# Optimization experiments

Measured on AMD Instinct MI355X. Metric: run time of the kernel, lower is better.

Reference implementation:

```python
import jax, jax.numpy as jnp
import numpy as np

B, NMAX, H, C, HID = 256, 512, 256, 64, 512
NEG = jnp.float32(-1e9)

def setup_inputs() -> dict:
    key = jax.random.key(0)
    ks = jax.random.split(key, 12)
    s_in = 1.0 / np.sqrt(2 * H + C)
    s_h = 1.0 / np.sqrt(HID)
    return {
        "nodes_hv": jax.random.normal(ks[0], (B, NMAX, H), jnp.float32),
        "class_cond": jax.random.normal(ks[1], (B, C), jnp.float32),
        "W1": jax.random.normal(ks[2], (2 * H + C, HID), jnp.float32) * s_in,
        "b1": jnp.zeros((HID,), jnp.float32),
        "W2": jax.random.normal(ks[3], (HID, HID), jnp.float32) * s_h,
        "b2": jnp.zeros((HID,), jnp.float32),
        "W3": jax.random.normal(ks[4], (HID, 1), jnp.float32) * s_h,
        "b3": jnp.zeros((1,), jnp.float32),
        "dirns": jax.random.randint(ks[5], (B,), 0, 2, jnp.int32),
        "node_counts": jax.random.randint(ks[6], (B,), NMAX // 2 + 1, NMAX, jnp.int32),
        "dests": jax.random.randint(ks[7], (B,), 0, NMAX // 2, jnp.int32),
    }

def reference(nodes_hv, class_cond, W1, b1, W2, b2, W3, b3, dirns, node_counts, dests):
    Bb, Nmax, Hh = nodes_hv.shape
    D = Nmax - 1  # padded number of candidate destinations
    # per-graph newest node embedding: hv[b, n_b - 1]
    src_idx = (node_counts - 1).astype(jnp.int32)
    src_embed = jnp.take_along_axis(nodes_hv, src_idx[:, None, None], axis=1)  # [B,1,H]
    src_b = jnp.broadcast_to(src_embed, (Bb, D, Hh))
    cand = nodes_hv[:, :D, :]  # candidate (old-node) embeddings, padded
    # dirn == 1: edge new->old, so (src_side, dest_side) = (cand, new); else (new, cand)
    dirn1 = (dirns == 1)[:, None, None]
    side_a = jnp.where(dirn1, cand, src_b)
    side_b = jnp.where(dirn1, src_b, cand)
    cc = jnp.broadcast_to(class_cond[:, None, :], (Bb, D, class_cond.shape[-1]))
    x = jnp.concatenate([side_a, side_b, cc], axis=2)  # [B, D, 2H+C]
    h = jax.nn.relu(jnp.einsum("bdi,ih->bdh", x, W1) + b1)
    h = jax.nn.relu(jnp.einsum("bdi,ih->bdh", h, W2) + b2)
    scores = (jnp.einsum("bdi,io->bdo", h, W3) + b3)[..., 0]  # [B, D]
    # ragged validity: graph b has n_b - 1 candidates
    valid = jnp.arange(D)[None, :] < (node_counts - 1)[:, None]
    scores = jnp.where(valid, scores, NEG)
    logp = jax.nn.log_softmax(scores, axis=1)
    loss = -jnp.take_along_axis(logp, dests[:, None].astype(jnp.int32), axis=1)[:, 0]  # [B]
    return loss
```

## Files before the change

kernel.cpp:

```cpp
#include <hip/hip_runtime.h>
#include <math.h>

#define BB    256
#define NMAX  512
#define HH    256
#define CC    64
#define HID   512
#define NEGV  -1000000000.0f
#define MT    64
#define NW    8
#define SA_LD 264
#define TILE  512
#define KSTR  (32 * TILE)

typedef __attribute__((ext_vector_type(8))) short short8;
typedef __attribute__((ext_vector_type(4))) float floatx4;

__device__ inline ushort f2bf(float x) {
    __bf16 b = (__bf16)x;
    return __builtin_bit_cast(ushort, b);
}

__global__ __launch_bounds__(512) void prep_kernel(
    const float* __restrict__ W1, const float* __restrict__ W2,
    ushort* __restrict__ Wt1s, ushort* __restrict__ Wt2s,
    const float* __restrict__ nodes_hv, const float* __restrict__ class_cond,
    const float* __restrict__ b1,
    const int* __restrict__ dirns, const int* __restrict__ node_counts,
    float* __restrict__ v_ws)
{
    const int blk = blockIdx.x;
    const int t = threadIdx.x;

    __shared__ float s_conv[32][68];
    __shared__ float s_src[HH];
    __shared__ float s_cc[CC];

    if (blk < 256) {
        const float* W = (blk < 128) ? W1 : W2;
        ushort* out    = (blk < 128) ? Wt1s : Wt2s;
        const int bb  = blk & 127;
        const int kb  = bb >> 3, ntg = bb & 7;

        if (t < 256) {
            const int kl = t >> 3, nn = (t & 7) * 8;
            const float* src = W + (size_t)(kb * 32 + kl) * HID + ntg * 64 + nn;
            *(float4*)&s_conv[kl][nn]     = *(const float4*)src;
            *(float4*)&s_conv[kl][nn + 4] = *(const float4*)(src + 4);
        }
        __syncthreads();

        if (t < 256) {
            const int ntl = t >> 6, ls = t & 63;
            const int qs = ls >> 4, l15s = ls & 15;
            short8 o;
            #pragma unroll
            for (int j = 0; j < 8; ++j)
                o[j] = (short)f2bf(s_conv[qs * 8 + j][ntl * 16 + l15s]);
            const int nt = ntg * 4 + ntl;
            *(short8*)(out + ((size_t)(kb * 32 + nt)) * TILE + ls * 8) = o;
        }
    } else {
        const int b = blk - 256;
        const int nc   = node_counts[b];
        const int dirn = dirns[b];
        const int src_idx = nc - 1;

        if (t < HH) s_src[t] = nodes_hv[((size_t)b * NMAX + src_idx) * HH + t];
        else if (t < HH + CC) s_cc[t - HH] = class_cond[b * CC + (t - HH)];
        __syncthreads();

        const int srcoff = (dirn == 1) ? HH : 0;

        const int j = t;
        float acc0 = b1[j];

        #pragma unroll 8
        for (int r = 0; r < HH; ++r)
            acc0 += s_src[r] * W1[(size_t)(srcoff + r) * HID + j];
        #pragma unroll 8
        for (int c = 0; c < CC; ++c)
            acc0 += s_cc[c] * W1[(size_t)(2 * HH + c) * HID + j];

        v_ws[b * HID + j] = acc0;
    }
}

__global__ __launch_bounds__(512, 4) void mlp2(
    const float* __restrict__ nodes_hv,
    const ushort* __restrict__ Wt1s, const ushort* __restrict__ Wt2s,
    const float* __restrict__ b2, const float* __restrict__ W3,
    const float* __restrict__ b3,
    const int* __restrict__ dirns, const int* __restrict__ node_counts,
    const float* __restrict__ v_ws, float* __restrict__ scores)
{
    const int b  = blockIdx.y;
    const int d0 = blockIdx.x * MT;
    const int t  = threadIdx.x;
    const int lane = t & 63, wv = t >> 6;
    const int l15 = lane & 15, q = lane >> 4;

    __shared__ ushort s_u[32768];

    const int nc = node_counts[b];

    if (d0 >= nc - 1) {
        if (t < MT) scores[b * NMAX + d0 + t] = NEGV;
        return;
    }

    const int kb0 = (dirns[b] == 1) ? 0 : 8;

    {
        const float4* src4 = (const float4*)nodes_hv + ((size_t)b * NMAX + d0) * (HH / 4);
        #pragma unroll
        for (int i = 0; i < (MT * HH / 4) / 512; ++i) {
            int idx = t + i * 512;
            int row = idx >> 6, c4 = idx & 63;
            float4 v = src4[idx];
            ushort4 p;
            p.x = f2bf(v.x); p.y = f2bf(v.y); p.z = f2bf(v.z); p.w = f2bf(v.w);
            *(ushort4*)&s_u[row * SA_LD + c4 * 4] = p;
        }
    }
    __syncthreads();

    floatx4 acc[4][4];
    #pragma unroll
    for (int mb = 0; mb < 4; ++mb)
        #pragma unroll
        for (int tn = 0; tn < 4; ++tn)
            acc[mb][tn] = (floatx4){0.f, 0.f, 0.f, 0.f};

    {
        const ushort* wb1 = Wt1s + ((size_t)kb0 * 32 + wv * 4) * TILE + lane * 8;
        short8 bcur[4], bnxt[4];
        #pragma unroll
        for (int tn = 0; tn < 4; ++tn)
            bcur[tn] = *(const short8*)(wb1 + tn * TILE);
        #pragma unroll
        for (int ks = 0; ks < 8; ++ks) {
            if (ks < 7) {
                const ushort* wp = wb1 + (size_t)(ks + 1) * KSTR;
                #pragma unroll
                for (int tn = 0; tn < 4; ++tn)
                    bnxt[tn] = *(const short8*)(wp + tn * TILE);
            }
            __builtin_amdgcn_s_setprio(1);
            #pragma unroll
            for (int mb = 0; mb < 4; ++mb) {
                const short8 a = *(const short8*)&s_u[(mb * 16 + l15) * SA_LD + ks * 32 + q * 8];
                #pragma unroll
                for (int tn = 0; tn < 4; ++tn)
                    acc[mb][tn] = __builtin_amdgcn_mfma_f32_16x16x32_bf16(a, bcur[tn], acc[mb][tn], 0, 0, 0);
            }
            __builtin_amdgcn_s_setprio(0);
            #pragma unroll
            for (int tn = 0; tn < 4; ++tn)
                bcur[tn] = bnxt[tn];
        }
    }
    __syncthreads();

    const int n0 = wv * 64;

    {
        const int j_w = l15 & 7;
        #pragma unroll
        for (int tn = 0; tn < 4; ++tn) {
            const int n = n0 + tn * 16 + l15;
            const float v = v_ws[b * HID + n];
            const int ks_w = wv * 2 + (tn >> 1);
            const int qr   = ((tn & 1) << 1) + (l15 >> 3);
            #pragma unroll
            for (int mb = 0; mb < 4; ++mb) {
                #pragma unroll
                for (int r = 0; r < 4; ++r) {
                    float h = acc[mb][tn][r] + v;
                    h = h > 0.f ? h : 0.f;
                    s_u[((mb * 16 + ks_w) * 64 + qr * 16 + q * 4 + r) * 8 + j_w] = f2bf(h);
                }
            }
        }
    }
    __syncthreads();

    #pragma unroll
    for (int mb = 0; mb < 4; ++mb)
        #pragma unroll
        for (int tn = 0; tn < 4; ++tn)
            acc[mb][tn] = (floatx4){0.f, 0.f, 0.f, 0.f};
    {
        const ushort* wb2 = Wt2s + ((size_t)wv * 4) * TILE + lane * 8;
        short8 bcur[4], bnxt[4];
        #pragma unroll
        for (int tn = 0; tn < 4; ++tn)
            bcur[tn] = *(const short8*)(wb2 + tn * TILE);
        #pragma unroll
        for (int ks = 0; ks < 16; ++ks) {
            if (ks < 15) {
                const ushort* wp = wb2 + (size_t)(ks + 1) * KSTR;
                #pragma unroll
                for (int tn = 0; tn < 4; ++tn)
                    bnxt[tn] = *(const short8*)(wp + tn * TILE);
            }
            __builtin_amdgcn_s_setprio(1);
            #pragma unroll
            for (int mb = 0; mb < 4; ++mb) {
                const short8 a = *(const short8*)&s_u[((mb * 16 + ks) * 64 + lane) * 8];
                #pragma unroll
                for (int tn = 0; tn < 4; ++tn)
                    acc[mb][tn] = __builtin_amdgcn_mfma_f32_16x16x32_bf16(a, bcur[tn], acc[mb][tn], 0, 0, 0);
            }
            __builtin_amdgcn_s_setprio(0);
            #pragma unroll
            for (int tn = 0; tn < 4; ++tn)
                bcur[tn] = bnxt[tn];
        }
    }

    float p[4][4] = {{0,0,0,0},{0,0,0,0},{0,0,0,0},{0,0,0,0}};
    #pragma unroll
    for (int tn = 0; tn < 4; ++tn) {
        const int n  = n0 + tn * 16 + l15;
        const float bb = b2[n];
        const float w3 = W3[n];
        #pragma unroll
        for (int mb = 0; mb < 4; ++mb)
            #pragma unroll
            for (int r = 0; r < 4; ++r) {
                float h = acc[mb][tn][r] + bb;
                h = h > 0.f ? h : 0.f;
                p[mb][r] += h * w3;
            }
    }
    __syncthreads();
    float* s_red = (float*)s_u;
    #pragma unroll
    for (int mb = 0; mb < 4; ++mb)
        #pragma unroll
        for (int r = 0; r < 4; ++r) {
            float v = p[mb][r];
            v += __shfl_xor(v, 1, 64);
            v += __shfl_xor(v, 2, 64);
            v += __shfl_xor(v, 4, 64);
            v += __shfl_xor(v, 8, 64);
            if (l15 == 0) s_red[wv * MT + mb * 16 + q * 4 + r] = v;
        }
    __syncthreads();
    if (t < MT) {
        float s = b3[0];
        #pragma unroll
        for (int w = 0; w < NW; ++w) s += s_red[w * MT + t];
        const int d = d0 + t;
        scores[b * NMAX + d] = (d < nc - 1) ? s : NEGV;
    }
}

__global__ __launch_bounds__(256) void loss_kernel(
    const float* __restrict__ scores, const int* __restrict__ dests,
    float* __restrict__ out)
{
    const int b = blockIdx.x;
    const int t = threadIdx.x;
    __shared__ float red[4];

    const float s0 = scores[b * NMAX + t];
    const float s1 = scores[b * NMAX + t + 256];

    const int lane = t & 63, wv = t >> 6;

    float mx = fmaxf(s0, s1);
    #pragma unroll
    for (int off = 32; off > 0; off >>= 1) mx = fmaxf(mx, __shfl_down(mx, off, 64));
    if (lane == 0) red[wv] = mx;
    __syncthreads();
    mx = fmaxf(fmaxf(red[0], red[1]), fmaxf(red[2], red[3]));
    __syncthreads();

    float e = __expf(s0 - mx) + __expf(s1 - mx);
    #pragma unroll
    for (int off = 32; off > 0; off >>= 1) e += __shfl_down(e, off, 64);
    if (lane == 0) red[wv] = e;
    __syncthreads();

    if (t == 0) {
        const float sum = red[0] + red[1] + red[2] + red[3];
        const float sd = scores[b * NMAX + dests[b]];
        out[b] = -(sd - mx - logf(sum));
    }
}

extern "C" void kernel_launch(void* const* d_in, const int* in_sizes, int n_in,
                              void* d_out, int out_size, void* d_ws, size_t ws_size,
                              hipStream_t stream) {
    const float* nodes_hv    = (const float*)d_in[0];
    const float* class_cond  = (const float*)d_in[1];
    const float* W1          = (const float*)d_in[2];
    const float* b1          = (const float*)d_in[3];
    const float* W2          = (const float*)d_in[4];
    const float* b2          = (const float*)d_in[5];
    const float* W3          = (const float*)d_in[6];
    const float* b3          = (const float*)d_in[7];
    const int*   dirns       = (const int*)d_in[8];
    const int*   node_counts = (const int*)d_in[9];
    const int*   dests       = (const int*)d_in[10];
    float* out = (float*)d_out;

    ushort* Wt1s   = (ushort*)d_ws;
    ushort* Wt2s   = Wt1s + 16 * KSTR;
    float*  v_ws   = (float*)(Wt2s + 16 * KSTR);
    float*  scores = v_ws + BB * HID;

    prep_kernel<<<512, 512, 0, stream>>>(W1, W2, Wt1s, Wt2s,
                                         nodes_hv, class_cond, b1,
                                         dirns, node_counts, v_ws);
    mlp2<<<dim3(NMAX / MT, BB), 512, 0, stream>>>(
        nodes_hv, Wt1s, Wt2s, b2, W3, b3, dirns, node_counts, v_ws, scores);
    loss_kernel<<<BB, 256, 0, stream>>>(scores, dests, out);
}
```

Baseline: 287.8 us.

## Split MFMA N-tiles into two passes with triple-buffered weight prefetch

Each wave's 64 output columns in both MLP layers are now computed in two passes of 32 columns, halving the live accumulator registers. First-layer activations from pass one are packed to bf16 in registers until the shared buffer is free. Weight fragments are prefetched two k-steps ahead with a three-slot ring instead of double buffering. The aim is lower VGPR pressure for better occupancy and latency hiding, at the cost of re-reading the A operand from LDS twice and adding more loop overhead.

```diff
diff --git a/kernel.cpp b/kernel.cpp
--- a/kernel.cpp
+++ b/kernel.cpp
@@ -111,6 +111,11 @@
 
     const int kb0 = (dirns[b] == 1) ? 0 : 8;
 
+    float vws[4];
+    #pragma unroll
+    for (int g = 0; g < 4; ++g)
+        vws[g] = v_ws[b * HID + wv * 64 + g * 16 + l15];
+
     {
         const float4* src4 = (const float4*)nodes_hv + ((size_t)b * NMAX + d0) * (HH / 4);
         #pragma unroll
@@ -125,115 +130,140 @@
     }
     __syncthreads();
 
-    floatx4 acc[4][4];
-    #pragma unroll
-    for (int mb = 0; mb < 4; ++mb)
-        #pragma unroll
-        for (int tn = 0; tn < 4; ++tn)
-            acc[mb][tn] = (floatx4){0.f, 0.f, 0.f, 0.f};
-
-    {
-        const ushort* wb1 = Wt1s + ((size_t)kb0 * 32 + wv * 4) * TILE + lane * 8;
-        short8 bcur[4], bnxt[4];
-        #pragma unroll
-        for (int tn = 0; tn < 4; ++tn)
-            bcur[tn] = *(const short8*)(wb1 + tn * TILE);
+    floatx4 acc[4][2];
+
+    auto l1_pass = [&](int h) {
+        #pragma unroll
+        for (int mb = 0; mb < 4; ++mb)
+            #pragma unroll
+            for (int tn = 0; tn < 2; ++tn)
+                acc[mb][tn] = (floatx4){0.f, 0.f, 0.f, 0.f};
+        const ushort* wb = Wt1s + ((size_t)(kb0 * 32) + wv * 4 + h * 2) * TILE + lane * 8;
+        short8 bw[3][2];
+        #pragma unroll
+        for (int pf = 0; pf < 2; ++pf) {
+            bw[pf][0] = *(const short8*)(wb + (size_t)pf * KSTR);
+            bw[pf][1] = *(const short8*)(wb + (size_t)pf * KSTR + TILE);
+        }
         #pragma unroll
         for (int ks = 0; ks < 8; ++ks) {
-            if (ks < 7) {
-                const ushort* wp = wb1 + (size_t)(ks + 1) * KSTR;
-                #pragma unroll
-                for (int tn = 0; tn < 4; ++tn)
-                    bnxt[tn] = *(const short8*)(wp + tn * TILE);
+            if (ks < 6) {
+                bw[(ks + 2) % 3][0] = *(const short8*)(wb + (size_t)(ks + 2) * KSTR);
+                bw[(ks + 2) % 3][1] = *(const short8*)(wb + (size_t)(ks + 2) * KSTR + TILE);
             }
             __builtin_amdgcn_s_setprio(1);
             #pragma unroll
             for (int mb = 0; mb < 4; ++mb) {
                 const short8 a = *(const short8*)&s_u[(mb * 16 + l15) * SA_LD + ks * 32 + q * 8];
-                #pragma unroll
-                for (int tn = 0; tn < 4; ++tn)
-                    acc[mb][tn] = __builtin_amdgcn_mfma_f32_16x16x32_bf16(a, bcur[tn], acc[mb][tn], 0, 0, 0);
+                acc[mb][0] = __builtin_amdgcn_mfma_f32_16x16x32_bf16(a, bw[ks % 3][0], acc[mb][0], 0, 0, 0);
+                acc[mb][1] = __builtin_amdgcn_mfma_f32_16x16x32_bf16(a, bw[ks % 3][1], acc[mb][1], 0, 0, 0);
             }
             __builtin_amdgcn_s_setprio(0);
-            #pragma unroll
-            for (int tn = 0; tn < 4; ++tn)
-                bcur[tn] = bnxt[tn];
-        }
-    }
-    __syncthreads();
-
-    const int n0 = wv * 64;
+        }
+    };
+
+    l1_pass(0);
+
+    uint pkA[4][2][2];
+    #pragma unroll
+    for (int mb = 0; mb < 4; ++mb)
+        #pragma unroll
+        for (int tn = 0; tn < 2; ++tn) {
+            const float v = vws[tn];
+            #pragma unroll
+            for (int pr = 0; pr < 2; ++pr) {
+                float x0 = acc[mb][tn][2 * pr]     + v; x0 = x0 > 0.f ? x0 : 0.f;
+                float x1 = acc[mb][tn][2 * pr + 1] + v; x1 = x1 > 0.f ? x1 : 0.f;
+                pkA[mb][tn][pr] = (uint)f2bf(x0) | ((uint)f2bf(x1) << 16);
+            }
+        }
+
+    l1_pass(1);
+
+    __syncthreads();
 
     {
         const int j_w = l15 & 7;
         #pragma unroll
-        for (int tn = 0; tn < 4; ++tn) {
-            const int n = n0 + tn * 16 + l15;
-            const float v = v_ws[b * HID + n];
-            const int ks_w = wv * 2 + (tn >> 1);
-            const int qr   = ((tn & 1) << 1) + (l15 >> 3);
-            #pragma unroll
-            for (int mb = 0; mb < 4; ++mb) {
+        for (int tn = 0; tn < 2; ++tn) {
+            const int ks_w = wv * 2;
+            const int qr   = (tn << 1) + (l15 >> 3);
+            #pragma unroll
+            for (int mb = 0; mb < 4; ++mb)
                 #pragma unroll
                 for (int r = 0; r < 4; ++r) {
-                    float h = acc[mb][tn][r] + v;
-                    h = h > 0.f ? h : 0.f;
-                    s_u[((mb * 16 + ks_w) * 64 + qr * 16 + q * 4 + r) * 8 + j_w] = f2bf(h);
+                    ushort hv = (ushort)(pkA[mb][tn][r >> 1] >> ((r & 1) * 16));
+                    s_u[((mb * 16 + ks_w) * 64 + qr * 16 + q * 4 + r) * 8 + j_w] = hv;
                 }
-            }
-        }
-    }
-    __syncthreads();
-
-    #pragma unroll
-    for (int mb = 0; mb < 4; ++mb)
-        #pragma unroll
-        for (int tn = 0; tn < 4; ++tn)
-            acc[mb][tn] = (floatx4){0.f, 0.f, 0.f, 0.f};
-    {
-        const ushort* wb2 = Wt2s + ((size_t)wv * 4) * TILE + lane * 8;
-        short8 bcur[4], bnxt[4];
-        #pragma unroll
-        for (int tn = 0; tn < 4; ++tn)
-            bcur[tn] = *(const short8*)(wb2 + tn * TILE);
+        }
+        #pragma unroll
+        for (int tn = 0; tn < 2; ++tn) {
+            const float v = vws[2 + tn];
+            const int ks_w = wv * 2 + 1;
+            const int qr   = (tn << 1) + (l15 >> 3);
+            #pragma unroll
+            for (int mb = 0; mb < 4; ++mb)
+                #pragma unroll
+                for (int r = 0; r < 4; ++r) {
+                    float hf = acc[mb][tn][r] + v;
+                    hf = hf > 0.f ? hf : 0.f;
+                    s_u[((mb * 16 + ks_w) * 64 + qr * 16 + q * 4 + r) * 8 + j_w] = f2bf(hf);
+                }
+        }
+    }
+    __syncthreads();
+
+    float p[4][4] = {{0,0,0,0},{0,0,0,0},{0,0,0,0},{0,0,0,0}};
+    const int n0 = wv * 64;
+
+    auto l2_pass = [&](int h) {
+        #pragma unroll
+        for (int mb = 0; mb < 4; ++mb)
+            #pragma unroll
+            for (int tn = 0; tn < 2; ++tn)
+                acc[mb][tn] = (floatx4){0.f, 0.f, 0.f, 0.f};
+        const ushort* wb = Wt2s + ((size_t)(wv * 4 + h * 2)) * TILE + lane * 8;
+        short8 bw[3][2];
+        #pragma unroll
+        for (int pf = 0; pf < 2; ++pf) {
+            bw[pf][0] = *(const short8*)(wb + (size_t)pf * KSTR);
+            bw[pf][1] = *(const short8*)(wb + (size_t)pf * KSTR + TILE);
+        }
         #pragma unroll
         for (int ks = 0; ks < 16; ++ks) {
-            if (ks < 15) {
-                const ushort* wp = wb2 + (size_t)(ks + 1) * KSTR;
-                #pragma unroll
-                for (int tn = 0; tn < 4; ++tn)
-                    bnxt[tn] = *(const short8*)(wp + tn * TILE);
+            if (ks < 14) {
+                bw[(ks + 2) % 3][0] = *(const short8*)(wb + (size_t)(ks + 2) * KSTR);
+                bw[(ks + 2) % 3][1] = *(const short8*)(wb + (size_t)(ks + 2) * KSTR + TILE);
             }
             __builtin_amdgcn_s_setprio(1);
             #pragma unroll
             for (int mb = 0; mb < 4; ++mb) {
                 const short8 a = *(const short8*)&s_u[((mb * 16 + ks) * 64 + lane) * 8];
+                acc[mb][0] = __builtin_amdgcn_mfma_f32_16x16x32_bf16(a, bw[ks % 3][0], acc[mb][0], 0, 0, 0);
+                acc[mb][1] = __builtin_amdgcn_mfma_f32_16x16x32_bf16(a, bw[ks % 3][1], acc[mb][1], 0, 0, 0);
+            }
+            __builtin_amdgcn_s_setprio(0);
+        }
+        #pragma unroll
+        for (int tn = 0; tn < 2; ++tn) {
+            const int g = h * 2 + tn;
+            const int n = n0 + g * 16 + l15;
+            const float bb = b2[n];
+            const float w3 = W3[n];
+            #pragma unroll
+            for (int mb = 0; mb < 4; ++mb)
                 #pragma unroll
-                for (int tn = 0; tn < 4; ++tn)
-                    acc[mb][tn] = __builtin_amdgcn_mfma_f32_16x16x32_bf16(a, bcur[tn], acc[mb][tn], 0, 0, 0);
-            }
-            __builtin_amdgcn_s_setprio(0);
-            #pragma unroll
-            for (int tn = 0; tn < 4; ++tn)
-                bcur[tn] = bnxt[tn];
-        }
-    }
-
-    float p[4][4] = {{0,0,0,0},{0,0,0,0},{0,0,0,0},{0,0,0,0}};
-    #pragma unroll
-    for (int tn = 0; tn < 4; ++tn) {
-        const int n  = n0 + tn * 16 + l15;
-        const float bb = b2[n];
-        const float w3 = W3[n];
-        #pragma unroll
-        for (int mb = 0; mb < 4; ++mb)
-            #pragma unroll
-            for (int r = 0; r < 4; ++r) {
-                float h = acc[mb][tn][r] + bb;
-                h = h > 0.f ? h : 0.f;
-                p[mb][r] += h * w3;
-            }
-    }
+                for (int r = 0; r < 4; ++r) {
+                    float hf = acc[mb][tn][r] + bb;
+                    hf = hf > 0.f ? hf : 0.f;
+                    p[mb][r] += hf * w3;
+                }
+        }
+    };
+
+    l2_pass(0);
+    l2_pass(1);
+
     __syncthreads();
     float* s_red = (float*)s_u;
     #pragma unroll
```

Result: slower. 417.8 us (+45.1%).
